# Optimization experiments

Hardware: AMD Instinct MI355X
Metric: run time of the kernel (lower is better)

Reference implementation:

```python
import jax, jax.numpy as jnp
import numpy as np

DIST_IND = 7.0        # disturbance_indicator
SLOPE_MIN, SLOPE_MAX = 0.0, 2.0
MAX_INTERCEPT = 100.0  # max_intercept / max_intercept_after_disturbance


def setup_inputs() -> dict:
    key = jax.random.key(0)
    k1, k2 = jax.random.split(key)
    # canopy-height-like values so year-over-year diffs < -7 occur (disturbances)
    out = jax.random.normal(k1, (8, 2, 30, 256, 256), dtype=jnp.float32) * 20.0 + 40.0
    target = jax.random.normal(k2, (8, 30, 256, 256), dtype=jnp.float32)
    return {"out": out, "target": target}


def _fit_segment(y, mask, x, n):
    """Masked OLS fit per pixel. y, mask, x: (B,Y,H,W); x is the local time index
    (pre-masked). n: (B,H,W) segment length. Returns fitted (B,Y,H,W), slope (B,H,W)."""
    n_safe = jnp.maximum(n, 1.0)
    mean_x = (x * mask).sum(1) / n_safe            # (B,H,W)
    mean_y = (y * mask).sum(1) / n_safe
    cov = ((x - mean_x[:, None]) * (y - mean_y[:, None]) * mask).sum(1)
    var = n * (n * n - 1.0) / 12.0                 # sum (x-mean_x)^2 for x=0..n-1
    slope = jnp.where(var > 0, cov / jnp.maximum(var, 1.0), 0.0)
    intercept = jnp.clip(mean_y - slope * mean_x, 0.0, MAX_INTERCEPT)
    fitted = jnp.clip(slope, SLOPE_MIN, SLOPE_MAX)[:, None] * x + intercept[:, None]
    return fitted, slope


def _forward(out, target):
    out0 = jax.lax.stop_gradient(out[:, 0])
    out1 = out[:, 1]
    B, Y, H, W = out0.shape
    # disturbance index: argmin over [-7, diff_1, ..., diff_{Y-1}] with entries 1, Y-1 zeroed
    diff = jnp.diff(out0, axis=1)
    diff = jnp.concatenate([jnp.full((B, 1, H, W), -DIST_IND, out0.dtype), diff], axis=1)
    diff = diff.at[:, 1].set(0.0).at[:, -1].set(0.0)  # full_disturbance_window=False
    d = jnp.argmin(diff, axis=1)                       # (B,H,W), first-min like torch
    t = jnp.arange(Y, dtype=out0.dtype)[None, :, None, None]
    df = d[:, None].astype(out0.dtype)                 # (B,1,H,W)
    mask_b = (t < df).astype(out0.dtype)               # before-disturbance timesteps
    mask_a = 1.0 - mask_b                              # from disturbance onward
    n_b = df[:, 0]
    n_a = Y - n_b
    fitted_b, _ = _fit_segment(out0, mask_b, t * mask_b, n_b)
    fitted_a, _ = _fit_segment(out0, mask_a, (t - df) * mask_a, n_a)
    fitted = jnp.where(mask_b > 0, fitted_b, fitted_a)  # piecewise fit, detached
    # use_l2=True; disturbance_factor == no_disturbance_factor == 1 -> plain mean
    loss = ((fitted - out1) ** 2).mean(axis=1).mean()
    return loss


def reference(out, target):
    return _forward(out, target)
```

## Files before the change

### kernel.cpp

```cpp
#include <hip/hip_runtime.h>

#define YDIM 30
#define HWSZ 65536
#define NBLK 2048
#define NTHR 256

__global__ __launch_bounds__(NTHR) void drl_main(const float* __restrict__ out,
                                                 float* __restrict__ partial) {
    const int tid = blockIdx.x * NTHR + threadIdx.x;
    const int b  = tid >> 16;
    const int hw = tid & (HWSZ - 1);

    const float* p0 = out + ((size_t)(b * 2) * YDIM) * HWSZ + hw;
    const float* p1 = p0 + (size_t)YDIM * HWSZ;

    float c0[YDIM];
#pragma unroll
    for (int y = 0; y < YDIM; ++y) c0[y] = p0[(size_t)y * HWSZ];

    float best = -7.0f;
    int d = 0;
#pragma unroll
    for (int y = 2; y < YDIM - 1; ++y) {
        float df = c0[y] - c0[y - 1];
        if (df < best) { best = df; d = y; }
    }
    const float fd = (float)d;

    float sy_b = 0.f, sy_a = 0.f;
#pragma unroll
    for (int y = 0; y < YDIM; ++y) {
        if (y < d) sy_b += c0[y];
        else       sy_a += c0[y];
    }
    const float nb = fd;
    const float na = (float)YDIM - fd;
    const float nsb = fmaxf(nb, 1.f);
    const float nsa = fmaxf(na, 1.f);
    const float mean_x_b = (fd * (fd - 1.f) * 0.5f) / nsb;
    const float mean_y_b = sy_b / nsb;
    const float mean_x_a = (na * (na - 1.f) * 0.5f) / nsa;
    const float mean_y_a = sy_a / nsa;

    float cov_b = 0.f, cov_a = 0.f;
#pragma unroll
    for (int y = 0; y < YDIM; ++y) {
        if (y < d) cov_b += ((float)y - mean_x_b) * (c0[y] - mean_y_b);
        else       cov_a += (((float)y - fd) - mean_x_a) * (c0[y] - mean_y_a);
    }
    const float var_b = nb * (nb * nb - 1.f) * (1.f / 12.f);
    const float var_a = na * (na * na - 1.f) * (1.f / 12.f);
    const float slope_b = (var_b > 0.f) ? cov_b / fmaxf(var_b, 1.f) : 0.f;
    const float slope_a = (var_a > 0.f) ? cov_a / fmaxf(var_a, 1.f) : 0.f;
    const float itc_b = fminf(fmaxf(mean_y_b - slope_b * mean_x_b, 0.f), 100.f);
    const float itc_a = fminf(fmaxf(mean_y_a - slope_a * mean_x_a, 0.f), 100.f);
    const float sc_b = fminf(fmaxf(slope_b, 0.f), 2.f);
    const float sc_a = fminf(fmaxf(slope_a, 0.f), 2.f);

    float acc = 0.f;
#pragma unroll
    for (int y = 0; y < YDIM; ++y) {
        float fit = (y < d) ? (sc_b * (float)y + itc_b)
                            : (sc_a * ((float)y - fd) + itc_a);
        float e = fit - p1[(size_t)y * HWSZ];
        acc += e * e;
    }

#pragma unroll
    for (int off = 32; off > 0; off >>= 1) acc += __shfl_down(acc, off, 64);

    __shared__ float wsum[NTHR / 64];
    const int lane = threadIdx.x & 63;
    const int wid  = threadIdx.x >> 6;
    if (lane == 0) wsum[wid] = acc;
    __syncthreads();
    if (threadIdx.x == 0) {
        partial[blockIdx.x] = wsum[0] + wsum[1] + wsum[2] + wsum[3];
    }
}

__global__ __launch_bounds__(NTHR) void drl_reduce(const float* __restrict__ partial,
                                                   float* __restrict__ outp) {
    double s = 0.0;
    for (int i = threadIdx.x; i < NBLK; i += NTHR) s += (double)partial[i];
    __shared__ double sm[NTHR];
    sm[threadIdx.x] = s;
    __syncthreads();
    for (int st = NTHR / 2; st > 0; st >>= 1) {
        if (threadIdx.x < st) sm[threadIdx.x] += sm[threadIdx.x + st];
        __syncthreads();
    }
    if (threadIdx.x == 0) {
        const double N = (double)(8 * YDIM) * (double)HWSZ;
        outp[0] = (float)(sm[0] / N);
    }
}

extern "C" void kernel_launch(void* const* d_in, const int* in_sizes, int n_in,
                              void* d_out, int out_size, void* d_ws, size_t ws_size,
                              hipStream_t stream) {
    const float* out_t = (const float*)d_in[0];
    float* partial = (float*)d_ws;
    float* loss    = (float*)d_out;

    drl_main<<<NBLK, NTHR, 0, stream>>>(out_t, partial);
    drl_reduce<<<1, NTHR, 0, stream>>>(partial, loss);
}
```

Measured before the change: 28.08 us.

## Vectorize pixel loads with float4 and compute segment OLS via single-pass running sums

After: 28.68 us. 2.1% more time.

```diff
diff --git a/kernel.cpp b/kernel.cpp
--- a/kernel.cpp
+++ b/kernel.cpp
@@ -1,82 +1,100 @@
 #include <hip/hip_runtime.h>
 
 #define YDIM 30
-#define HWSZ 65536
-#define NBLK 2048
+#define PLANE4 16384
 #define NTHR 256
+#define NBLK 512
 
-__global__ __launch_bounds__(NTHR) void drl_main(const float* __restrict__ out,
+__global__ __launch_bounds__(NTHR) void drl_main(const float4* __restrict__ out,
                                                  float* __restrict__ partial) {
-    const int tid = blockIdx.x * NTHR + threadIdx.x;
-    const int b  = tid >> 16;
-    const int hw = tid & (HWSZ - 1);
+    const int g = blockIdx.x * NTHR + threadIdx.x;
+    const int b = g >> 14;
+    const int hw4 = g & 16383;
 
-    const float* p0 = out + ((size_t)(b * 2) * YDIM) * HWSZ + hw;
-    const float* p1 = p0 + (size_t)YDIM * HWSZ;
+    const float4* p0 = out + (size_t)b * (2 * YDIM * PLANE4) + hw4;
+    const float4* p1 = p0 + YDIM * PLANE4;
 
-    float c0[YDIM];
-#pragma unroll
-    for (int y = 0; y < YDIM; ++y) c0[y] = p0[(size_t)y * HWSZ];
+    float run_s [4] = {0.f,0.f,0.f,0.f};
+    float run_sx[4] = {0.f,0.f,0.f,0.f};
+    float snap_s [4] = {0.f,0.f,0.f,0.f};
+    float snap_sx[4] = {0.f,0.f,0.f,0.f};
+    float best[4] = {-7.f,-7.f,-7.f,-7.f};
+    float fd  [4] = {0.f,0.f,0.f,0.f};
+    float prev[4];
 
-    float best = -7.0f;
-    int d = 0;
-#pragma unroll
-    for (int y = 2; y < YDIM - 1; ++y) {
-        float df = c0[y] - c0[y - 1];
-        if (df < best) { best = df; d = y; }
-    }
-    const float fd = (float)d;
-
-    float sy_b = 0.f, sy_a = 0.f;
 #pragma unroll
     for (int y = 0; y < YDIM; ++y) {
-        if (y < d) sy_b += c0[y];
-        else       sy_a += c0[y];
+        float4 v = p0[y * PLANE4];
+        float cur[4] = {v.x, v.y, v.z, v.w};
+        if (y >= 2 && y <= YDIM - 2) {
+#pragma unroll
+            for (int c = 0; c < 4; ++c) {
+                float df = cur[c] - prev[c];
+                bool lt = df < best[c];
+                best[c]    = lt ? df         : best[c];
+                fd[c]      = lt ? (float)y   : fd[c];
+                snap_s[c]  = lt ? run_s[c]   : snap_s[c];
+                snap_sx[c] = lt ? run_sx[c]  : snap_sx[c];
+            }
+        }
+#pragma unroll
+        for (int c = 0; c < 4; ++c) {
+            run_s[c]  += cur[c];
+            run_sx[c]  = fmaf((float)y, cur[c], run_sx[c]);
+            prev[c]    = cur[c];
+        }
     }
-    const float nb = fd;
-    const float na = (float)YDIM - fd;
-    const float nsb = fmaxf(nb, 1.f);
-    const float nsa = fmaxf(na, 1.f);
-    const float mean_x_b = (fd * (fd - 1.f) * 0.5f) / nsb;
-    const float mean_y_b = sy_b / nsb;
-    const float mean_x_a = (na * (na - 1.f) * 0.5f) / nsa;
-    const float mean_y_a = sy_a / nsa;
 
-    float cov_b = 0.f, cov_a = 0.f;
+    float sc_b[4], itc_b[4], sc_a[4], itc_a[4];
+#pragma unroll
+    for (int c = 0; c < 4; ++c) {
+        float nb  = fd[c];
+        float na  = (float)YDIM - nb;
+        float nsb = fmaxf(nb, 1.f);
+        float sy_b  = snap_s[c];
+        float sxy_b = snap_sx[c];
+        float sy_a  = run_s[c]  - sy_b;
+        float sxy_a = (run_sx[c] - snap_sx[c]) - nb * sy_a;
+        float mxb = nb * (nb - 1.f) * 0.5f / nsb;
+        float myb = sy_b / nsb;
+        float mxa = na * (na - 1.f) * 0.5f / na;
+        float mya = sy_a / na;
+        float cov_b = sxy_b - mxb * sy_b;
+        float cov_a = sxy_a - mxa * sy_a;
+        float var_b = nb * (nb * nb - 1.f) * (1.f / 12.f);
+        float var_a = na * (na * na - 1.f) * (1.f / 12.f);
+        float slope_b = (var_b > 0.f) ? cov_b / fmaxf(var_b, 1.f) : 0.f;
+        float slope_a = (var_a > 0.f) ? cov_a / fmaxf(var_a, 1.f) : 0.f;
+        itc_b[c] = fminf(fmaxf(myb - slope_b * mxb, 0.f), 100.f);
+        itc_a[c] = fminf(fmaxf(mya - slope_a * mxa, 0.f), 100.f);
+        sc_b[c]  = fminf(fmaxf(slope_b, 0.f), 2.f);
+        sc_a[c]  = fminf(fmaxf(slope_a, 0.f), 2.f);
+    }
+
+    float acc[4] = {0.f,0.f,0.f,0.f};
 #pragma unroll
     for (int y = 0; y < YDIM; ++y) {
-        if (y < d) cov_b += ((float)y - mean_x_b) * (c0[y] - mean_y_b);
-        else       cov_a += (((float)y - fd) - mean_x_a) * (c0[y] - mean_y_a);
+        float4 v = p1[y * PLANE4];
+        float t1[4] = {v.x, v.y, v.z, v.w};
+#pragma unroll
+        for (int c = 0; c < 4; ++c) {
+            float xf  = (float)y;
+            float fb  = fmaf(sc_b[c], xf,          itc_b[c]);
+            float fa  = fmaf(sc_a[c], xf - fd[c],  itc_a[c]);
+            float fit = (xf < fd[c]) ? fb : fa;
+            float e   = fit - t1[c];
+            acc[c]    = fmaf(e, e, acc[c]);
+        }
     }
-    const float var_b = nb * (nb * nb - 1.f) * (1.f / 12.f);
-    const float var_a = na * (na * na - 1.f) * (1.f / 12.f);
-    const float slope_b = (var_b > 0.f) ? cov_b / fmaxf(var_b, 1.f) : 0.f;
-    const float slope_a = (var_a > 0.f) ? cov_a / fmaxf(var_a, 1.f) : 0.f;
-    const float itc_b = fminf(fmaxf(mean_y_b - slope_b * mean_x_b, 0.f), 100.f);
-    const float itc_a = fminf(fmaxf(mean_y_a - slope_a * mean_x_a, 0.f), 100.f);
-    const float sc_b = fminf(fmaxf(slope_b, 0.f), 2.f);
-    const float sc_a = fminf(fmaxf(slope_a, 0.f), 2.f);
-
-    float acc = 0.f;
-#pragma unroll
-    for (int y = 0; y < YDIM; ++y) {
-        float fit = (y < d) ? (sc_b * (float)y + itc_b)
-                            : (sc_a * ((float)y - fd) + itc_a);
-        float e = fit - p1[(size_t)y * HWSZ];
-        acc += e * e;
-    }
+    float a = (acc[0] + acc[1]) + (acc[2] + acc[3]);
 
 #pragma unroll
-    for (int off = 32; off > 0; off >>= 1) acc += __shfl_down(acc, off, 64);
-
+    for (int off = 32; off > 0; off >>= 1) a += __shfl_down(a, off, 64);
     __shared__ float wsum[NTHR / 64];
-    const int lane = threadIdx.x & 63;
-    const int wid  = threadIdx.x >> 6;
-    if (lane == 0) wsum[wid] = acc;
+    if ((threadIdx.x & 63) == 0) wsum[threadIdx.x >> 6] = a;
     __syncthreads();
-    if (threadIdx.x == 0) {
-        partial[blockIdx.x] = wsum[0] + wsum[1] + wsum[2] + wsum[3];
-    }
+    if (threadIdx.x == 0)
+        partial[blockIdx.x] = (wsum[0] + wsum[1]) + (wsum[2] + wsum[3]);
 }
 
 __global__ __launch_bounds__(NTHR) void drl_reduce(const float* __restrict__ partial,
@@ -91,7 +109,7 @@
         __syncthreads();
     }
     if (threadIdx.x == 0) {
-        const double N = (double)(8 * YDIM) * (double)HWSZ;
+        const double N = (double)(8 * YDIM) * 65536.0;
         outp[0] = (float)(sm[0] / N);
     }
 }
@@ -99,7 +117,7 @@
 extern "C" void kernel_launch(void* const* d_in, const int* in_sizes, int n_in,
                               void* d_out, int out_size, void* d_ws, size_t ws_size,
                               hipStream_t stream) {
-    const float* out_t = (const float*)d_in[0];
+    const float4* out_t = (const float4*)d_in[0];
     float* partial = (float*)d_ws;
     float* loss    = (float*)d_out;
 
```
